# Optimization experiments

Hardware: AMD Instinct MI355X
Metric: run time of the kernel (lower is better)

Reference implementation:

```python
import jax, jax.numpy as jnp
import numpy as np

H = 2048      # hidden_size
I = 4096      # intermediate_size
N = 128       # ssm state_size
HEADS = 64
P = 64        # head_dim
K = 4         # conv kernel
CHUNK = 256
DT_MIN, DT_MAX = 0.0, 100.0
EPS = 1e-5


def segsum(x):
    # x: (..., T) -> (..., T, T) with out[i, j] = sum_{k=j+1..i} x[k], -inf above diag
    T = x.shape[-1]
    cs = jnp.cumsum(x, axis=-1)
    d = cs[..., :, None] - cs[..., None, :]
    mask = jnp.tril(jnp.ones((T, T), dtype=bool))
    return jnp.where(mask, d, -jnp.inf)


def setup_inputs() -> dict:
    key = jax.random.key(0)
    ks = jax.random.split(key, 8)
    return {
        "hidden_states": jax.random.normal(ks[0], (2, 4096, H), jnp.float32),
        "in_proj_w": jax.random.normal(ks[1], (2 * (I + N) + HEADS, H), jnp.float32) * 0.02,
        "conv_w": jax.random.normal(ks[2], (I + 2 * N, 1, K), jnp.float32) * 0.2,
        "conv_b": jax.random.normal(ks[3], (I + 2 * N,), jnp.float32) * 0.02,
        "dt_bias": jax.random.uniform(ks[4], (HEADS,), jnp.float32),
        "A_log": jnp.log(jax.random.uniform(ks[5], (HEADS,), jnp.float32, 1.0, 16.0)),
        "D": jnp.ones((HEADS,), jnp.float32),
        "norm_w": jnp.ones((I,), jnp.float32),
        "out_proj_w": jax.random.normal(ks[6], (H, I), jnp.float32) * 0.02,
    }


def reference(hidden_states, in_proj_w, conv_w, conv_b, dt_bias, A_log, D, norm_w, out_proj_w):
    b, l, _ = hidden_states.shape
    # in_proj -> [z (I), xBC (I+2N), dt (HEADS)]  (d_mlp == 0 with these dims)
    zxbcdt = hidden_states @ in_proj_w.T
    z, xBC, dt = jnp.split(zxbcdt, [I, I + (I + 2 * N)], axis=-1)

    # causal depthwise conv1d + SiLU
    conv = jax.lax.conv_general_dilated(
        xBC.transpose(0, 2, 1), conv_w, (1,), [(K - 1, 0)],
        dimension_numbers=("NCH", "OIH", "NCH"), feature_group_count=I + 2 * N)
    xBC = jax.nn.silu((conv + conv_b[None, :, None]).transpose(0, 2, 1))
    x, B, C = jnp.split(xBC, [I, I + N], axis=-1)

    A = -jnp.exp(A_log)                                        # (h,)
    dt = jnp.clip(jax.nn.softplus(dt + dt_bias), DT_MIN, DT_MAX)  # (b,l,h)

    # SSD chunked scan (groups = 1 for B/C)
    X = x.reshape(b, l, HEADS, P) * dt[..., None]              # x * dt
    Adt = dt * A                                               # (b,l,h)
    c = l // CHUNK
    Xc = X.reshape(b, c, CHUNK, HEADS, P)
    Bc = B.reshape(b, c, CHUNK, N)
    Cc = C.reshape(b, c, CHUNK, N)
    Ac = Adt.reshape(b, c, CHUNK, HEADS).transpose(0, 3, 1, 2)  # (b,h,c,cl)
    A_cum = jnp.cumsum(Ac, axis=-1)

    # intra-chunk (diagonal) contribution
    L = jnp.exp(segsum(Ac))                                    # (b,h,c,cl,cl)
    Y_diag = jnp.einsum("bcln,bcsn,bhcls,bcshp->bclhp", Cc, Bc, L, Xc)

    # chunk states and inter-chunk recurrence
    decay_states = jnp.exp(A_cum[..., -1:] - A_cum)            # (b,h,c,cl)
    states = jnp.einsum("bcln,bhcl,bclhp->bchpn", Bc, decay_states, Xc)
    states = jnp.concatenate([jnp.zeros_like(states[:, :1]), states], axis=1)
    chunk_A = jnp.pad(A_cum[..., -1], ((0, 0), (0, 0), (1, 0)))  # (b,h,c+1)
    decay_chunk = jnp.exp(segsum(chunk_A))                     # (b,h,c+1,c+1)
    new_states = jnp.einsum("bhzc,bchpn->bzhpn", decay_chunk, states)
    prev_states = new_states[:, :-1]                           # (b,c,h,p,n)

    Y_off = jnp.einsum("bcln,bchpn,bhcl->bclhp", Cc, prev_states, jnp.exp(A_cum))
    y = (Y_diag + Y_off).reshape(b, l, HEADS, P)
    y = y + x.reshape(b, l, HEADS, P) * D[None, None, :, None]  # skip (D term)
    y = y.reshape(b, l, I)

    # gated RMSNorm (norm_before_gate=True): normalize, gate by silu(z), scale
    yf = y.astype(jnp.float32)
    yf = yf * jax.lax.rsqrt(jnp.mean(yf * yf, axis=-1, keepdims=True) + EPS)
    yf = yf * jax.nn.silu(z.astype(jnp.float32))
    y = (norm_w * yf).astype(hidden_states.dtype)

    return y @ out_proj_w.T
```

## Files before the change

### kernel.cpp

```cpp
#include <hip/hip_runtime.h>

typedef unsigned short u16;
typedef __attribute__((ext_vector_type(8))) short bfx8;
typedef __attribute__((ext_vector_type(4))) float f32x4;
typedef __attribute__((ext_vector_type(4))) unsigned short u16x4;

__device__ __forceinline__ float bf2f(u16 u){ return __builtin_bit_cast(float, (unsigned)u << 16); }
__device__ __forceinline__ u16 f2bf(float f){
  unsigned u = __builtin_bit_cast(unsigned, f);
  return (u16)((u + 0x7fffu + ((u >> 16) & 1u)) >> 16);
}

__device__ __forceinline__ void gload_lds16(const void* g, void* l){
  __builtin_amdgcn_global_load_lds((const __attribute__((address_space(1))) void*)g,
                                   (__attribute__((address_space(3))) void*)l, 16, 0, 0);
}

__global__ __launch_bounds__(256) void cvt_kernel(const float* __restrict__ in, u16* __restrict__ out, int n4){
  int i = blockIdx.x * 256 + threadIdx.x;
  if (i >= n4) return;
  f32x4 v = *(const f32x4*)&in[(long)i * 4];
  u16x4 o = { f2bf(v[0]), f2bf(v[1]), f2bf(v[2]), f2bf(v[3]) };
  *(u16x4*)&out[(long)i * 4] = o;
}

__global__ __launch_bounds__(256) void cvt2_kernel(const float* __restrict__ a, u16* __restrict__ oa, int na4,
                                                   const float* __restrict__ b2, u16* __restrict__ ob, int nb4){
  int i = blockIdx.x * 256 + threadIdx.x;
  const float* src; u16* dst; int idx;
  if (i < na4){ src = a; dst = oa; idx = i; }
  else { idx = i - na4; if (idx >= nb4) return; src = b2; dst = ob; }
  f32x4 v = *(const f32x4*)&src[(long)idx * 4];
  u16x4 o = { f2bf(v[0]), f2bf(v[1]), f2bf(v[2]), f2bf(v[3]) };
  *(u16x4*)&dst[(long)idx * 4] = o;
}

template<int F32OUT>
__global__ __launch_bounds__(512, 2)
void gemm256(const u16* __restrict__ A, const u16* __restrict__ W,
             void* __restrict__ out0, void* __restrict__ out1,
             int K, int ld0, int ld1, int nsplit)
{
  __shared__ __align__(16) u16 SA[2][16384];
  __shared__ __align__(16) u16 SB[2][16384];
  const int tid = threadIdx.x;
  const int wid = tid >> 6, lane = tid & 63;
  const int wr = wid >> 2, wc = wid & 3;
  const int bm = blockIdx.x, bn = blockIdx.y;
  const int rr = lane & 15, kg = lane >> 4;
  const int NT = K >> 6;

  const int srow = tid >> 3;
  const int ssw = ((tid & 7) * 16) ^ ((srow & 7) << 4);
  const u16* gA = A + ((long)bm * 256 + srow) * K + (ssw >> 1);
  const u16* gB = W + ((long)bn * 256 + srow) * K + (ssw >> 1);
  const long r64 = (long)64 * K;
  const int dst = tid * 8;

#define STAGE_A(t, ht) { const u16* s_ = gA + (long)(ht) * 2 * r64 + ((t) << 6); \
    gload_lds16(s_,       &SA[(t) & 1][(ht) * 8192 + dst]); \
    gload_lds16(s_ + r64, &SA[(t) & 1][(ht) * 8192 + 4096 + dst]); }
#define STAGE_B(t, ht) { const u16* s_ = gB + (long)(ht) * 2 * r64 + ((t) << 6); \
    gload_lds16(s_,       &SB[(t) & 1][(ht) * 8192 + dst]); \
    gload_lds16(s_ + r64, &SB[(t) & 1][(ht) * 8192 + 4096 + dst]); }

  const int swr = (rr & 7) << 4;
  const int ca0 = ((kg * 16) ^ swr) >> 1;
  const int ca1 = ((64 + kg * 16) ^ swr) >> 1;
  int bA[8], bB[4];
#pragma unroll
  for (int j = 0; j < 8; j++) bA[j] = ((2 * j + wr) * 16 + rr) * 64;
#pragma unroll
  for (int i = 0; i < 4; i++) bB[i] = ((4 * i + wc) * 16 + rr) * 64;

  f32x4 acc[8][4] = {};

  STAGE_A(0, 0); STAGE_A(0, 1); STAGE_B(0, 0); STAGE_B(0, 1);
  if (NT > 1) STAGE_A(1, 0);
  asm volatile("s_waitcnt vmcnt(2)" ::: "memory");
  asm volatile("s_barrier" ::: "memory");

  for (int u = 0; u < NT; ++u){
    const int p = u & 1;
    bfx8 bf[4][2];
#pragma unroll
    for (int k = 0; k < 4; ++k){
      bfx8 af[2][2];
#pragma unroll
      for (int jj = 0; jj < 2; jj++){
        const int base = bA[2 * k + jj];
        af[jj][0] = *(const bfx8*)&SA[p][base + ca0];
        af[jj][1] = *(const bfx8*)&SA[p][base + ca1];
      }
      if (k == 0){
#pragma unroll
        for (int i = 0; i < 4; i++){
          bf[i][0] = *(const bfx8*)&SB[p][bB[i] + ca0];
          bf[i][1] = *(const bfx8*)&SB[p][bB[i] + ca1];
        }
        if (u + 1 < NT) { STAGE_B(u + 1, 0); STAGE_B(u + 1, 1); }
      }
      else if (k == 1) { if (u + 1 < NT) STAGE_A(u + 1, 1); }
      else if (k == 3) {
        if (u + 2 < NT)      { STAGE_A(u + 2, 0); asm volatile("s_waitcnt vmcnt(2)" ::: "memory"); }
        else if (u + 1 < NT) { asm volatile("s_waitcnt vmcnt(0)" ::: "memory"); }
      }
      asm volatile("s_barrier" ::: "memory");
      __builtin_amdgcn_s_setprio(1);
#pragma unroll
      for (int jj = 0; jj < 2; jj++)
#pragma unroll
        for (int i = 0; i < 4; i++){
          acc[2 * k + jj][i] = __builtin_amdgcn_mfma_f32_16x16x32_bf16(af[jj][0], bf[i][0], acc[2 * k + jj][i], 0, 0, 0);
          acc[2 * k + jj][i] = __builtin_amdgcn_mfma_f32_16x16x32_bf16(af[jj][1], bf[i][1], acc[2 * k + jj][i], 0, 0, 0);
        }
      __builtin_amdgcn_s_setprio(0);
    }
  }
#undef STAGE_A
#undef STAGE_B

  int bn2 = bn; void* op = out0; int ldo = ld0;
  if (bn >= nsplit){ bn2 = bn - nsplit; op = out1; ldo = ld1; }
  const int r4b = (lane >> 4) * 4;
#pragma unroll
  for (int j = 0; j < 8; j++)
#pragma unroll
    for (int i = 0; i < 4; i++)
#pragma unroll
      for (int r4 = 0; r4 < 4; r4++){
        long row = (long)bm * 256 + (2 * j + wr) * 16 + r4b + r4;
        long col = (long)bn2 * 256 + (4 * i + wc) * 16 + rr;
        long idx = row * ldo + col;
        if (F32OUT) ((float*)op)[idx] = acc[j][i][r4];
        else        ((u16*)op)[idx]  = f2bf(acc[j][i][r4]);
      }
}

__global__ __launch_bounds__(256) void dt_kernel(const float* __restrict__ hs, const float* __restrict__ w,
                                                 const float* __restrict__ dt_bias, float* __restrict__ dtp){
  __shared__ float hsS[32][66];
  __shared__ float wS[64][66];
  const int tid = threadIdx.x;
  const int j = tid & 63, rgrp = tid >> 6;
  const long row0 = (long)blockIdx.x * 32;
  const int srow = tid >> 3, sc0 = (tid & 7) * 8;
  const int wrow = tid >> 2, wc0 = (tid & 3) * 16;
  const float* hsg = hs + (row0 + srow) * 2048 + sc0;
  const float* wg  = w + (long)(8448 + wrow) * 2048 + wc0;

  f32x4 acc[8] = {};
  for (int k0 = 0; k0 < 2048; k0 += 64){
    *(f32x4*)&hsS[srow][sc0]     = *(const f32x4*)&hsg[k0];
    *(f32x4*)&hsS[srow][sc0 + 4] = *(const f32x4*)&hsg[k0 + 4];
#pragma unroll
    for (int q = 0; q < 4; q++)
      *(f32x4*)&wS[wrow][wc0 + q * 4] = *(const f32x4*)&wg[k0 + q * 4];
    __syncthreads();
#pragma unroll
    for (int kk = 0; kk < 64; kk += 4){
      f32x4 wv = *(const f32x4*)&wS[j][kk];
#pragma unroll
      for (int r = 0; r < 8; r++){
        f32x4 hv = *(const f32x4*)&hsS[rgrp * 8 + r][kk];
        acc[r] += hv * wv;
      }
    }
    __syncthreads();
  }
  float bias = dt_bias[j];
#pragma unroll
  for (int r = 0; r < 8; r++){
    float x = acc[r][0] + acc[r][1] + acc[r][2] + acc[r][3] + bias;
    float sp = (x > 20.f) ? x : log1pf(expf(x));
    sp = fminf(fmaxf(sp, 0.f), 100.f);
    dtp[(row0 + rgrp * 8 + r) * 64 + j] = sp;
  }
}

__global__ __launch_bounds__(64) void acum_kernel(const float* __restrict__ dtp, const float* __restrict__ A_log,
                                                  float* __restrict__ acum, float* __restrict__ suma){
  int bid = blockIdx.x;
  int c = bid & 15, h = (bid >> 4) & 63, b = bid >> 10;
  int lane = threadIdx.x;
  float Ah = -expf(A_log[h]);
  long base = ((long)(b * 4096 + c * 256)) * 64 + h;
  float v[4]; float s = 0.f;
#pragma unroll
  for (int i = 0; i < 4; i++){ float adt = dtp[base + (lane * 4 + i) * 64] * Ah; s += adt; v[i] = s; }
  float tot = s, run = s;
  for (int off = 1; off < 64; off <<= 1){ float u = __shfl_up(run, off); if (lane >= off) run += u; }
  float excl = run - tot;
  long ob = (long)bid * 256 + lane * 4;
#pragma unroll
  for (int i = 0; i < 4; i++) acum[ob + i] = excl + v[i];
  if (lane == 63) suma[bid] = run;
}

__global__ __launch_bounds__(256) void conv_kernel(const u16* __restrict__ xbc, const float* __restrict__ cw,
                                                   const float* __restrict__ cb,
                                                   u16* __restrict__ xact,
                                                   u16* __restrict__ bmat, u16* __restrict__ cmat){
  int pb = blockIdx.x;
  int l0 = (pb & 1023) * 4;
  long pos0 = ((long)(pb >> 10) << 12) + l0;
  for (int cg = threadIdx.x; cg < 544; cg += 256){
    int ch = cg * 8;
    f32x4 cwv[8];
#pragma unroll
    for (int t = 0; t < 8; t++) cwv[t] = *(const f32x4*)&cw[(ch + t) * 4];
    float cbv[8];
#pragma unroll
    for (int t = 0; t < 8; t++) cbv[t] = cb[ch + t];
    bfx8 rr[7];
    bfx8 zz = {};
    rr[0] = (l0 >= 3) ? *(const bfx8*)&xbc[(pos0 - 3) * 4352 + ch] : zz;
    rr[1] = (l0 >= 2) ? *(const bfx8*)&xbc[(pos0 - 2) * 4352 + ch] : zz;
    rr[2] = (l0 >= 1) ? *(const bfx8*)&xbc[(pos0 - 1) * 4352 + ch] : zz;
#pragma unroll
    for (int q = 0; q < 4; q++) rr[3 + q] = *(const bfx8*)&xbc[(pos0 + q) * 4352 + ch];
#pragma unroll
    for (int li = 0; li < 4; li++){
      bfx8 o;
#pragma unroll
      for (int t = 0; t < 8; t++){
        float a = cbv[t] + cwv[t][0] * bf2f((u16)rr[li][t])     + cwv[t][1] * bf2f((u16)rr[li + 1][t])
                         + cwv[t][2] * bf2f((u16)rr[li + 2][t]) + cwv[t][3] * bf2f((u16)rr[li + 3][t]);
        float val = a / (1.f + expf(-a));
        o[t] = (short)f2bf(val);
      }
      long pos = pos0 + li;
      if (ch < 4096)      *(bfx8*)&xact[pos * 4096 + ch] = o;
      else if (ch < 4224) *(bfx8*)&bmat[pos * 128 + ch - 4096] = o;
      else                *(bfx8*)&cmat[pos * 128 + ch - 4224] = o;
    }
  }
}

__global__ __launch_bounds__(256) void bt_transpose(const u16* __restrict__ bmat, u16* __restrict__ bmatT){
  __shared__ u16 T[128 * 136];
  int bx = blockIdx.x;
  int b = bx >> 5, lt = bx & 31;
  int l0 = lt * 128;
  int tid = threadIdx.x;
  for (int idx = tid; idx < 2048; idx += 256){
    int lrow = idx >> 4, ns = (idx & 15) * 8;
    *(bfx8*)&T[lrow * 136 + ns] = *(const bfx8*)&bmat[((long)b * 4096 + l0 + lrow) * 128 + ns];
  }
  __syncthreads();
  for (int idx = tid; idx < 2048; idx += 256){
    int nrow = idx >> 4, ls = (idx & 15) * 8;
    bfx8 o;
#pragma unroll
    for (int j = 0; j < 8; j++) o[j] = (short)T[(ls + j) * 136 + nrow];
    *(bfx8*)&bmatT[(long)b * 524288 + (long)nrow * 4096 + l0 + ls] = o;
  }
}

__global__ __launch_bounds__(256, 4) void states_kernel(const u16* __restrict__ xact, const u16* __restrict__ bmatT,
                                                        const float* __restrict__ acum, const float* __restrict__ suma,
                                                        const float* __restrict__ dtp, u16* __restrict__ stR){
  __shared__ __align__(16) u16 XdT[64 * 264];
  __shared__ float fac[256];
  int bid = blockIdx.x;
  int h = bid & 63, c = (bid >> 6) & 15, b = bid >> 10;
  int tid = threadIdx.x;
  long rowbase = (long)b * 4096 + c * 256;
  long aco = ((long)((b * 64 + h) * 16 + c)) * 256;
  float sA = suma[(b * 64 + h) * 16 + c];
  fac[tid] = dtp[(rowbase + tid) * 64 + h] * expf(sA - acum[aco + tid]);
  __syncthreads();
  char* xb = (char*)XdT;
  for (int idx = tid; idx < 2048; idx += 256){
    int l = idx >> 3, ps = (idx & 7) * 8;
    int key = (idx & 7) << 4;
    bfx8 xv = *(const bfx8*)&xact[(rowbase + l) * 4096 + h * 64 + ps];
#pragma unroll
    for (int j = 0; j < 8; j++)
      *(u16*)(xb + ((((ps + j) * 264 + l) * 2) ^ key)) = f2bf(bf2f((u16)xv[j]) * fac[l]);
  }
  __syncthreads();
  int wid = tid >> 6, lane = tid & 63;
  int rr = lane & 15, ko = (lane >> 4) * 8;
  const u16* btb = bmatT + (long)b * 524288 + c * 256;
  const int arow = wid * 16 + rr;
  const int akey = ((arow >> 3) & 7) << 4;
  f32x4 acc[8] = {};
#pragma unroll
  for (int ks = 0; ks < 8; ks++){
    bfx8 a = *(const bfx8*)(xb + (((arow * 264 + ks * 32 + ko) * 2) ^ akey));
#pragma unroll
    for (int nt = 0; nt < 8; nt++){
      bfx8 bb = *(const bfx8*)&btb[(long)(nt * 16 + rr) * 4096 + ks * 32 + ko];
      acc[nt] = __builtin_amdgcn_mfma_f32_16x16x32_bf16(a, bb, acc[nt], 0, 0, 0);
    }
  }
  long ob = (long)bid * 8192;
#pragma unroll
  for (int nt = 0; nt < 8; nt++)
#pragma unroll
    for (int r4 = 0; r4 < 4; r4++){
      int p = wid * 16 + (lane >> 4) * 4 + r4;
      stR[ob + p * 128 + nt * 16 + rr] = f2bf(acc[nt][r4]);
    }
}

__global__ __launch_bounds__(256) void scan_kernel(u16* stR, const float* __restrict__ suma){
  int g = blockIdx.x;
  int s = g & 7, bh = g >> 3;
  int b = bh >> 6, h = bh & 63;
  int tid = threadIdx.x;
  long off0 = (long)s * 1024 + tid * 4;
  f32x4 R = {};
  for (int c = 0; c < 16; c++){
    long base = ((long)((b * 16 + c) * 64 + h)) * 8192 + off0;
    float sc = expf(suma[(b * 64 + h) * 16 + c]);
    u16x4 e4 = *(const u16x4*)&stR[base];
    u16x4 o = { f2bf(R[0]), f2bf(R[1]), f2bf(R[2]), f2bf(R[3]) };
    *(u16x4*)&stR[base] = o;
#pragma unroll
    for (int t = 0; t < 4; t++) R[t] = sc * R[t] + bf2f(e4[t]);
  }
}

__global__ __launch_bounds__(256, 3) void ydiag_kernel(const u16* __restrict__ cmat, const u16* __restrict__ bmat,
                                                       const u16* xact,
                                                       const u16* __restrict__ rbuf, const float* __restrict__ acum,
                                                       const float* __restrict__ dtp,
                                                       const float* __restrict__ Dv, u16* ybuf){
  __shared__ __align__(16) u16 XdTq[64 * 72];
  __shared__ __align__(16) u16 Sb[4][64 * 36];
  __shared__ float acL[256];
  __shared__ float dtl[256];
  int bid = blockIdx.x;
  int h = bid & 63, c = (bid >> 6) & 15, b = bid >> 10;
  int tid = threadIdx.x, wid = tid >> 6, lane = tid & 63;
  long rowbase = (long)b * 4096 + c * 256;
  long aco = ((long)((b * 64 + h) * 16 + c)) * 256;
  acL[tid] = acum[aco + tid];
  dtl[tid] = dtp[(rowbase + tid) * 64 + h];
  __syncthreads();

  int rr = lane & 15, ko = (lane >> 4) * 8;
  f32x4 acc[4][4] = {};

  long rb = (long)bid * 8192;
#pragma unroll
  for (int kk = 0; kk < 4; kk++){
    bfx8 cf[4];
#pragma unroll
    for (int lt = 0; lt < 4; lt++)
      cf[lt] = *(const bfx8*)&cmat[(rowbase + wid * 64 + lt * 16 + rr) * 128 + kk * 32 + ko];
#pragma unroll
    for (int pt = 0; pt < 4; pt++){
      bfx8 bb = *(const bfx8*)&rbuf[rb + (pt * 16 + rr) * 128 + kk * 32 + ko];
#pragma unroll
      for (int lt = 0; lt < 4; lt++) acc[lt][pt] = __builtin_amdgcn_mfma_f32_16x16x32_bf16(cf[lt], bb, acc[lt][pt], 0, 0, 0);
    }
  }
#pragma unroll
  for (int lt = 0; lt < 4; lt++)
#pragma unroll
    for (int r4 = 0; r4 < 4; r4++){
      float e = expf(acL[wid * 64 + lt * 16 + (lane >> 4) * 4 + r4]);
#pragma unroll
      for (int pt = 0; pt < 4; pt++) acc[lt][pt][r4] *= e;
    }

  char* xqb = (char*)XdTq;
  const int nsp = 2 * (wid + 1);
  for (int q = 0; q < 4; q++){
    __syncthreads();
    for (int idx = tid; idx < 512; idx += 256){
      int lq = idx >> 3, ps = (idx & 7) * 8;
      int key = (idx & 7) << 4;
      int l = q * 64 + lq;
      bfx8 xv = *(const bfx8*)&xact[(rowbase + l) * 4096 + h * 64 + ps];
#pragma unroll
      for (int j = 0; j < 8; j++)
        *(u16*)(xqb + ((((ps + j) * 72 + lq) * 2) ^ key)) = f2bf(bf2f((u16)xv[j]) * dtl[l]);
    }
    __syncthreads();
#pragma unroll
    for (int sub = 0; sub < 2; sub++){
      int sp = q * 2 + sub;
      if (sp >= nsp) continue;
      int s0 = sp * 32;
      f32x4 sacc[2][4] = {};
#pragma unroll
      for (int kk = 0; kk < 4; kk++){
        bfx8 cf[4];
#pragma unroll
        for (int lt = 0; lt < 4; lt++)
          cf[lt] = *(const bfx8*)&cmat[(rowbase + wid * 64 + lt * 16 + rr) * 128 + kk * 32 + ko];
#pragma unroll
        for (int st = 0; st < 2; st++){
          bfx8 bb = *(const bfx8*)&bmat[(rowbase + s0 + st * 16 + rr) * 128 + kk * 32 + ko];
#pragma unroll
          for (int lt = 0; lt < 4; lt++) sacc[st][lt] = __builtin_amdgcn_mfma_f32_16x16x32_bf16(cf[lt], bb, sacc[st][lt], 0, 0, 0);
        }
      }
#pragma unroll
      for (int st = 0; st < 2; st++)
#pragma unroll
        for (int lt = 0; lt < 4; lt++)
#pragma unroll
          for (int r4 = 0; r4 < 4; r4++){
            int lrow = wid * 64 + lt * 16 + (lane >> 4) * 4 + r4;
            int scol = s0 + st * 16 + rr;
            float vv = (scol <= lrow) ? sacc[st][lt][r4] * expf(acL[lrow] - acL[scol]) : 0.f;
            Sb[wid][(lt * 16 + (lane >> 4) * 4 + r4) * 36 + st * 16 + rr] = f2bf(vv);
          }
      asm volatile("s_waitcnt lgkmcnt(0)" ::: "memory");
      __builtin_amdgcn_sched_barrier(0);
#pragma unroll
      for (int lt = 0; lt < 4; lt++){
        bfx8 a1 = *(const bfx8*)&Sb[wid][(lt * 16 + rr) * 36 + ko];
#pragma unroll
        for (int pt = 0; pt < 4; pt++){
          int prow = pt * 16 + rr;
          bfx8 bb = *(const bfx8*)(xqb + (((prow * 72 + sub * 32 + ko) * 2) ^ (((prow >> 3) & 7) << 4)));
          acc[lt][pt] = __builtin_amdgcn_mfma_f32_16x16x32_bf16(a1, bb, acc[lt][pt], 0, 0, 0);
        }
      }
    }
  }
  float Dh = Dv[h];
#pragma unroll
  for (int lt = 0; lt < 4; lt++)
#pragma unroll
    for (int pt = 0; pt < 4; pt++)
#pragma unroll
      for (int r4 = 0; r4 < 4; r4++){
        int lrow = wid * 64 + lt * 16 + (lane >> 4) * 4 + r4;
        int pcol = pt * 16 + rr;
        long gi = (rowbase + lrow) * 4096 + h * 64 + pcol;
        ybuf[gi] = f2bf(acc[lt][pt][r4] + bf2f(xact[gi]) * Dh);
      }
}

__global__ __launch_bounds__(256) void rms_kernel(const u16* ybuf, const u16* zbuf,
                                                  const float* __restrict__ norm_w, u16* ynorm){
  __shared__ float red[4];
  long row = blockIdx.x;
  int tid = threadIdx.x;
  long yb = row * 4096 + tid * 16;
  bfx8 v0 = *(const bfx8*)&ybuf[yb];
  bfx8 v1 = *(const bfx8*)&ybuf[yb + 8];
  float vals[16];
#pragma unroll
  for (int t = 0; t < 8; t++){ vals[t] = bf2f((u16)v0[t]); vals[8 + t] = bf2f((u16)v1[t]); }
  float ss = 0.f;
#pragma unroll
  for (int t = 0; t < 16; t++) ss += vals[t] * vals[t];
#pragma unroll
  for (int off = 32; off >= 1; off >>= 1) ss += __shfl_xor(ss, off);
  if ((tid & 63) == 0) red[tid >> 6] = ss;
  __syncthreads();
  float rs = rsqrtf((red[0] + red[1] + red[2] + red[3]) * (1.f / 4096.f) + 1e-5f);
  bfx8 z0 = *(const bfx8*)&zbuf[yb];
  bfx8 z1 = *(const bfx8*)&zbuf[yb + 8];
  bfx8 o0, o1;
#pragma unroll
  for (int t = 0; t < 16; t++){
    float zv = bf2f((u16)(t < 8 ? z0[t] : z1[t - 8]));
    float g = zv / (1.f + expf(-zv));
    u16 r = f2bf(vals[t] * rs * norm_w[tid * 16 + t] * g);
    if (t < 8) o0[t] = (short)r; else o1[t - 8] = (short)r;
  }
  *(bfx8*)&ynorm[yb] = o0;
  *(bfx8*)&ynorm[yb + 8] = o1;
}

extern "C" void kernel_launch(void* const* d_in, const int* in_sizes, int n_in,
                              void* d_out, int out_size, void* d_ws, size_t ws_size,
                              hipStream_t stream){
  const float* hs   = (const float*)d_in[0];
  const float* inw  = (const float*)d_in[1];
  const float* cw   = (const float*)d_in[2];
  const float* cb   = (const float*)d_in[3];
  const float* dtb  = (const float*)d_in[4];
  const float* alog = (const float*)d_in[5];
  const float* Dv   = (const float*)d_in[6];
  const float* nw   = (const float*)d_in[7];
  const float* outw = (const float*)d_in[8];

  const size_t REQ = 147857408ULL;
  if (ws_size < REQ){
    hipMemsetAsync(d_out, 0x42, (size_t)out_size * 4, stream);
    return;
  }
  char* ws = (char*)d_ws;
  u16*   hsb  = (u16*)  (ws + 0L);
  u16*   wbi  = (u16*)  (ws + 33554432L);
  u16*   xbc  = (u16*)  (ws + 68157440L);
  u16*   xact = (u16*)  (ws + 0L);
  u16*   stR  = (u16*)  (ws + 68157440L);
  u16*   wbo  = (u16*)  (ws + 101711872L);
  u16*   bmatT= (u16*)  (ws + 118489088L);
  float* dtp  = (float*)(ws + 139460608L);
  float* acum = (float*)(ws + 141557760L);
  float* suma = (float*)(ws + 143654912L);
  u16*   bmat = (u16*)  (ws + 143663104L);
  u16*   cmat = (u16*)  (ws + 145760256L);
  u16*   zbuf = (u16*)  d_out;

  cvt2_kernel<<<33280, 256, 0, stream>>>(hs, hsb, 4194304, inw, wbi, 4325376);
  gemm256<0><<<dim3(32, 33), 512, 0, stream>>>(hsb, wbi, zbuf, xbc, 2048, 4096, 4352, 16);
  dt_kernel<<<256, 256, 0, stream>>>(hs, inw, dtb, dtp);
  acum_kernel<<<2048, 64, 0, stream>>>(dtp, alog, acum, suma);
  conv_kernel<<<2048, 256, 0, stream>>>(xbc, cw, cb, xact, bmat, cmat);
  cvt_kernel<<<8192, 256, 0, stream>>>(outw, wbo, 2097152);
  bt_transpose<<<64, 256, 0, stream>>>(bmat, bmatT);
  states_kernel<<<2048, 256, 0, stream>>>(xact, bmatT, acum, suma, dtp, stR);
  scan_kernel<<<1024, 256, 0, stream>>>(stR, suma);
  ydiag_kernel<<<2048, 256, 0, stream>>>(cmat, bmat, xact, stR, acum, dtp, Dv, xact);
  rms_kernel<<<8192, 256, 0, stream>>>(xact, zbuf, nw, xact);
  gemm256<1><<<dim3(32, 8), 512, 0, stream>>>(xact, wbo, d_out, d_out, 4096, 2048, 2048, 999);
}
```

Measured before the change: 993.0 us.

## Precompute head-independent C·Bᵀ per chunk once instead of per head in ydiag

The C·Bᵀ product within each chunk does not depend on the head. Before this change, each of the 64 per-head ydiag blocks recomputed it with MFMAs. A new cbt_kernel computes it once per (batch, chunk) into an fp32 workspace buffer G. ydiag then loads G rows directly into the MFMA A-operand layout, applying the decay mask in registers, which removes the LDS staging buffer and lets launch bounds rise to four blocks per CU. The cost is an extra launch and 64 MB of fp32 G reads across all heads, which replace on-chip recomputation.

```diff
diff --git a/kernel.cpp b/kernel.cpp
--- a/kernel.cpp
+++ b/kernel.cpp
@@ -255,6 +255,38 @@
     for (int j = 0; j < 8; j++) o[j] = (short)T[(ls + j) * 136 + nrow];
     *(bfx8*)&bmatT[(long)b * 524288 + (long)nrow * 4096 + l0 + ls] = o;
   }
+}
+
+__global__ __launch_bounds__(256) void cbt_kernel(const u16* __restrict__ cmat, const u16* __restrict__ bmat,
+                                                  float* __restrict__ G){
+  int bid = blockIdx.x;
+  int ss = bid & 3, bc = bid >> 2;
+  int b = bc >> 4, c = bc & 15;
+  long rowbase = (long)b * 4096 + c * 256;
+  int tid = threadIdx.x, wid = tid >> 6, lane = tid & 63;
+  int rr = lane & 15, ko = (lane >> 4) * 8;
+  f32x4 acc[4][4] = {};
+#pragma unroll
+  for (int kk = 0; kk < 4; kk++){
+    bfx8 cf[4], bf[4];
+#pragma unroll
+    for (int lt = 0; lt < 4; lt++) cf[lt] = *(const bfx8*)&cmat[(rowbase + wid * 64 + lt * 16 + rr) * 128 + kk * 32 + ko];
+#pragma unroll
+    for (int st = 0; st < 4; st++) bf[st] = *(const bfx8*)&bmat[(rowbase + ss * 64 + st * 16 + rr) * 128 + kk * 32 + ko];
+#pragma unroll
+    for (int lt = 0; lt < 4; lt++)
+#pragma unroll
+      for (int st = 0; st < 4; st++)
+        acc[lt][st] = __builtin_amdgcn_mfma_f32_16x16x32_bf16(cf[lt], bf[st], acc[lt][st], 0, 0, 0);
+  }
+  long gb2 = (long)bc * 65536;
+#pragma unroll
+  for (int lt = 0; lt < 4; lt++)
+#pragma unroll
+    for (int st = 0; st < 4; st++)
+#pragma unroll
+      for (int r4 = 0; r4 < 4; r4++)
+        G[gb2 + (long)(wid * 64 + lt * 16 + (lane >> 4) * 4 + r4) * 256 + ss * 64 + st * 16 + rr] = acc[lt][st][r4];
 }
 
 __global__ __launch_bounds__(256, 4) void states_kernel(const u16* __restrict__ xact, const u16* __restrict__ bmatT,
@@ -323,13 +355,12 @@
   }
 }
 
-__global__ __launch_bounds__(256, 3) void ydiag_kernel(const u16* __restrict__ cmat, const u16* __restrict__ bmat,
+__global__ __launch_bounds__(256, 4) void ydiag_kernel(const u16* __restrict__ cmat, const float* __restrict__ G,
                                                        const u16* xact,
                                                        const u16* __restrict__ rbuf, const float* __restrict__ acum,
                                                        const float* __restrict__ dtp,
                                                        const float* __restrict__ Dv, u16* ybuf){
   __shared__ __align__(16) u16 XdTq[64 * 72];
-  __shared__ __align__(16) u16 Sb[4][64 * 36];
   __shared__ float acL[256];
   __shared__ float dtl[256];
   int bid = blockIdx.x;
@@ -368,6 +399,7 @@
     }
 
   char* xqb = (char*)XdTq;
+  const long gb2 = (long)((b * 16 + c)) * 65536;
   const int nsp = 2 * (wid + 1);
   for (int q = 0; q < 4; q++){
     __syncthreads();
@@ -386,36 +418,25 @@
       int sp = q * 2 + sub;
       if (sp >= nsp) continue;
       int s0 = sp * 32;
-      f32x4 sacc[2][4] = {};
-#pragma unroll
-      for (int kk = 0; kk < 4; kk++){
-        bfx8 cf[4];
-#pragma unroll
-        for (int lt = 0; lt < 4; lt++)
-          cf[lt] = *(const bfx8*)&cmat[(rowbase + wid * 64 + lt * 16 + rr) * 128 + kk * 32 + ko];
-#pragma unroll
-        for (int st = 0; st < 2; st++){
-          bfx8 bb = *(const bfx8*)&bmat[(rowbase + s0 + st * 16 + rr) * 128 + kk * 32 + ko];
-#pragma unroll
-          for (int lt = 0; lt < 4; lt++) sacc[st][lt] = __builtin_amdgcn_mfma_f32_16x16x32_bf16(cf[lt], bb, sacc[st][lt], 0, 0, 0);
+#pragma unroll
+      for (int lt = 0; lt < 4; lt++){
+        int lrow = wid * 64 + lt * 16 + rr;
+        float eL = acL[lrow];
+        f32x4 g0 = *(const f32x4*)&G[gb2 + (long)lrow * 256 + s0 + ko];
+        f32x4 g1 = *(const f32x4*)&G[gb2 + (long)lrow * 256 + s0 + ko + 4];
+        bfx8 a1;
+#pragma unroll
+        for (int j = 0; j < 4; j++){
+          int s = s0 + ko + j;
+          float sc = (s <= lrow) ? expf(eL - acL[s]) : 0.f;
+          a1[j] = (short)f2bf(g0[j] * sc);
         }
-      }
-#pragma unroll
-      for (int st = 0; st < 2; st++)
-#pragma unroll
-        for (int lt = 0; lt < 4; lt++)
-#pragma unroll
-          for (int r4 = 0; r4 < 4; r4++){
-            int lrow = wid * 64 + lt * 16 + (lane >> 4) * 4 + r4;
-            int scol = s0 + st * 16 + rr;
-            float vv = (scol <= lrow) ? sacc[st][lt][r4] * expf(acL[lrow] - acL[scol]) : 0.f;
-            Sb[wid][(lt * 16 + (lane >> 4) * 4 + r4) * 36 + st * 16 + rr] = f2bf(vv);
-          }
-      asm volatile("s_waitcnt lgkmcnt(0)" ::: "memory");
-      __builtin_amdgcn_sched_barrier(0);
-#pragma unroll
-      for (int lt = 0; lt < 4; lt++){
-        bfx8 a1 = *(const bfx8*)&Sb[wid][(lt * 16 + rr) * 36 + ko];
+#pragma unroll
+        for (int j = 0; j < 4; j++){
+          int s = s0 + ko + 4 + j;
+          float sc = (s <= lrow) ? expf(eL - acL[s]) : 0.f;
+          a1[4 + j] = (short)f2bf(g1[j] * sc);
+        }
 #pragma unroll
         for (int pt = 0; pt < 4; pt++){
           int prow = pt * 16 + rr;
@@ -498,6 +519,7 @@
   u16*   stR  = (u16*)  (ws + 68157440L);
   u16*   wbo  = (u16*)  (ws + 101711872L);
   u16*   bmatT= (u16*)  (ws + 118489088L);
+  float* Gbuf = (float*)(ws + 120586240L);
   float* dtp  = (float*)(ws + 139460608L);
   float* acum = (float*)(ws + 141557760L);
   float* suma = (float*)(ws + 143654912L);
@@ -512,9 +534,10 @@
   conv_kernel<<<2048, 256, 0, stream>>>(xbc, cw, cb, xact, bmat, cmat);
   cvt_kernel<<<8192, 256, 0, stream>>>(outw, wbo, 2097152);
   bt_transpose<<<64, 256, 0, stream>>>(bmat, bmatT);
+  cbt_kernel<<<128, 256, 0, stream>>>(cmat, bmat, Gbuf);
   states_kernel<<<2048, 256, 0, stream>>>(xact, bmatT, acum, suma, dtp, stR);
   scan_kernel<<<1024, 256, 0, stream>>>(stR, suma);
-  ydiag_kernel<<<2048, 256, 0, stream>>>(cmat, bmat, xact, stR, acum, dtp, Dv, xact);
+  ydiag_kernel<<<2048, 256, 0, stream>>>(cmat, Gbuf, xact, stR, acum, dtp, Dv, xact);
   rms_kernel<<<8192, 256, 0, stream>>>(xact, zbuf, nw, xact);
   gemm256<1><<<dim3(32, 8), 512, 0, stream>>>(xact, wbo, d_out, d_out, 4096, 2048, 2048, 999);
 }
```

Result: faster. 903.9 us (-9.0%).
